# Kernel tuning notes

Hardware: AMD Instinct MI355X
Metric: run time of the kernel (lower is better)

## Reference

```python
import jax, jax.numpy as jnp
import numpy as np

B, P1, P2 = 16, 25, 24          # batch, patch-grid rows (+cls row), cols
E0, E1, E2 = 8, 8, 16           # 3-way factorized embed dim (total 1024)
H1, H2, H3 = 2, 2, 4            # 3-way head split (16 heads)
X, Y, Z = E0 // H1, E1 // H2, E2 // H3   # per-head factor dims (4,4,4)
SCALE = float((X * Y * Z) ** -0.5)        # head_dim = 64


def _tcl(x, w0, w1, w2, b):
    # Tensor Contraction Layer: mode-wise linear maps on the 3 embed modes.
    return jnp.einsum('bpqxyz,ax,cy,dz->bpqacd', x, w0, w1, w2) + b


def setup_inputs() -> dict:
    key = jax.random.key(0)
    ks = jax.random.split(key, 17)
    inp = {"x": jax.random.normal(ks[0], (B, P1, P2, E0, E1, E2), jnp.float32)}
    i = 1
    for nm in ("q", "k", "v", "o"):
        inp[f"{nm}_w0"] = jax.random.normal(ks[i], (E0, E0), jnp.float32) * (E0 ** -0.5); i += 1
        inp[f"{nm}_w1"] = jax.random.normal(ks[i], (E1, E1), jnp.float32) * (E1 ** -0.5); i += 1
        inp[f"{nm}_w2"] = jax.random.normal(ks[i], (E2, E2), jnp.float32) * (E2 ** -0.5); i += 1
        inp[f"{nm}_b"] = jax.random.normal(ks[i], (E0, E1, E2), jnp.float32) * 0.02; i += 1
    return inp


def _split_heads(t):
    t = t.reshape(B, P1, P2, X, H1, Y, H2, Z, H3)
    return t.transpose(0, 1, 2, 4, 6, 8, 3, 5, 7)


def reference(x,
              q_w0, q_w1, q_w2, q_b,
              k_w0, k_w1, k_w2, k_b,
              v_w0, v_w1, v_w2, v_b,
              o_w0, o_w1, o_w2, o_b):
    q = _tcl(x, q_w0, q_w1, q_w2, q_b)
    k = _tcl(x, k_w0, k_w1, k_w2, k_b)
    v = _tcl(x, v_w0, v_w1, v_w2, v_b)
    Q, K, V = _split_heads(q), _split_heads(k), _split_heads(v)
    # scores over all (p1,p2) x (m,n) token pairs, per (h1,h2,h3) head
    attn = jnp.einsum('bpqdefxyz,bmndefxyz->bdefpqmn', Q, K) * SCALE
    a = attn.reshape(B, H1, H2, H3, P1, P2, P1 * P2)
    a = jax.nn.softmax(a, axis=-1).reshape(attn.shape)
    out = jnp.einsum('bdefpqmn,bmndefxyz->bdefpqxyz', a, V)
    # b h1 h2 h3 p q x y z -> b p q (x h1)(y h2)(z h3)
    out = out.transpose(0, 4, 5, 6, 1, 7, 2, 8, 3).reshape(B, P1, P2, E0, E1, E2)
    return _tcl(out, o_w0, o_w1, o_w2, o_b)
```

## Files before the change

### kernel.cpp

```cpp
#include <hip/hip_runtime.h>

#define S   600
#define NB  16
#define NH  16
#define HD  64
#define QSCALE 0.18033688011112042f

#define LDT 20

typedef _Float16 f16x8 __attribute__((ext_vector_type(8)));
typedef __fp16 fp16x2 __attribute__((ext_vector_type(2)));
typedef float f32x4 __attribute__((ext_vector_type(4)));
typedef float f32x16 __attribute__((ext_vector_type(16)));
typedef int v2i __attribute__((ext_vector_type(2)));
typedef unsigned int u32;

__global__ __launch_bounds__(256) void tcl_qkv_kernel(
    const float* __restrict__ x,
    const float* __restrict__ qw0, const float* __restrict__ qw1,
    const float* __restrict__ qw2, const float* __restrict__ qb,
    const float* __restrict__ kw0, const float* __restrict__ kw1,
    const float* __restrict__ kw2, const float* __restrict__ kb,
    const float* __restrict__ vw0, const float* __restrict__ vw1,
    const float* __restrict__ vw2, const float* __restrict__ vb,
    _Float16* __restrict__ Qh, _Float16* __restrict__ Kh,
    _Float16* __restrict__ Vh)
{
  __shared__ __align__(16) float t1s[4][64 * LDT];
  __shared__ __align__(16) float t2s[4][64 * LDT];

  const int tid = threadIdx.x;
  const int wv = tid >> 6, lane = tid & 63;
  const int tok = blockIdx.x * 4 + wv;
  const int b = tok / S, t = tok - b * S;
  const int q = lane >> 3, zp = lane & 7;
  float* __restrict__ t1 = t1s[wv];
  float* __restrict__ t2 = t2s[wv];

  float2 xc[8];
  #pragma unroll
  for (int xx = 0; xx < 8; ++xx)
    xc[xx] = *(const float2*)&x[(size_t)tok * 1024 + xx * 128 + q * 16 + zp * 2];

  const int xs = lane >> 4;
  const int h1 = (lane >> 3) & 1;
  const int cc = lane & 7;
  const int ys = cc >> 1, h2 = cc & 1;

  const float* W0[3] = {qw0, kw0, vw0};
  const float* W1[3] = {qw1, kw1, vw1};
  const float* W2[3] = {qw2, kw2, vw2};
  const float* BB[3] = {qb, kb, vb};
  _Float16* OUT[3] = {Qh, Kh, Vh};

  #pragma unroll
  for (int p = 0; p < 3; ++p) {
    const float* __restrict__ w0 = W0[p];
    const float* __restrict__ w1 = W1[p];
    const float* __restrict__ w2 = W2[p];
    const float* __restrict__ bb = BB[p];
    _Float16* __restrict__ op = OUT[p];

    #pragma unroll
    for (int a = 0; a < 8; ++a) {
      float2 r = make_float2(0.f, 0.f);
      #pragma unroll
      for (int xx = 0; xx < 8; ++xx) {
        const float w = w0[a * 8 + xx];
        r.x = fmaf(w, xc[xx].x, r.x);
        r.y = fmaf(w, xc[xx].y, r.y);
      }
      *(float2*)&t1[(a * 8 + q) * LDT + zp * 2] = r;
    }
    __builtin_amdgcn_wave_barrier();

    float2 t1r[8];
    #pragma unroll
    for (int y = 0; y < 8; ++y)
      t1r[y] = *(float2*)&t1[(q * 8 + y) * LDT + zp * 2];
    #pragma unroll
    for (int c = 0; c < 8; ++c) {
      float2 r = make_float2(0.f, 0.f);
      #pragma unroll
      for (int y = 0; y < 8; ++y) {
        const float w = w1[c * 8 + y];
        r.x = fmaf(w, t1r[y].x, r.x);
        r.y = fmaf(w, t1r[y].y, r.y);
      }
      *(float2*)&t2[(q * 8 + c) * LDT + zp * 2] = r;
    }
    __builtin_amdgcn_wave_barrier();

    float t2r[16];
    #pragma unroll
    for (int k = 0; k < 4; ++k)
      *(float4*)&t2r[k * 4] = *(float4*)&t2[lane * LDT + k * 4];
    float bias[16];
    #pragma unroll
    for (int k = 0; k < 4; ++k)
      *(float4*)&bias[k * 4] = *(const float4*)&bb[lane * 16 + k * 4];
    float o[16];
    #pragma unroll
    for (int d = 0; d < 16; ++d) {
      float acc = 0.f;
      #pragma unroll
      for (int j = 0; j < 16; ++j)
        acc = fmaf(w2[d * 16 + j], t2r[j], acc);
      o[d] = acc + bias[d];
    }
    const float sc = (p == 0) ? QSCALE : 1.0f;
    #pragma unroll
    for (int h3 = 0; h3 < 4; ++h3) {
      union { _Float16 hh[4]; uint2 u; } pk;
      #pragma unroll
      for (int z = 0; z < 4; ++z)
        pk.hh[z] = (_Float16)(o[4 * z + h3] * sc);
      const int head = h1 * 8 + h2 * 4 + h3;
      *(uint2*)&op[((size_t)((b * NH + head) * S + t)) * HD + xs * 16 + ys * 4]
          = pk.u;
    }
    __builtin_amdgcn_wave_barrier();
  }
}

__global__ __launch_bounds__(256) void vtrans_kernel(
    const _Float16* __restrict__ Vh, _Float16* __restrict__ Vt)
{
  __shared__ __align__(16) _Float16 tile[64 * 64];
  const int tid = threadIdx.x;
  const int tt = blockIdx.x, h = blockIdx.y, b = blockIdx.z;
  const size_t rbase = (size_t)(b * NH + h) * S * HD;
  const size_t wbase = (size_t)(b * NH + h) * HD * S;
  const int t0 = tt * 64;

  #pragma unroll
  for (int hp = 0; hp < 2; ++hp) {
    const int u = hp * 256 + tid;
    const int r = u >> 3, ch = u & 7;
    f16x8 v = {0, 0, 0, 0, 0, 0, 0, 0};
    if (t0 + r < S) v = *(const f16x8*)&Vh[rbase + (size_t)(t0 + r) * HD + ch * 8];
    *(f16x8*)&tile[r * 64 + ((ch ^ ((r ^ (r >> 3)) & 7)) * 8)] = v;
  }
  __syncthreads();
  #pragma unroll
  for (int hp = 0; hp < 2; ++hp) {
    const int w = hp * 256 + tid;
    const int d = w >> 3, tc = w & 7;
    if (t0 + tc * 8 + 8 <= S) {
      const int cd = d >> 3;
      union { _Float16 hh[8]; f16x8 v; } g;
      #pragma unroll
      for (int e = 0; e < 8; ++e) {
        const int r = tc * 8 + e;
        g.hh[e] = tile[r * 64 + ((cd ^ ((r ^ (r >> 3)) & 7)) * 8) + (d & 7)];
      }
      *(f16x8*)&Vt[wbase + (size_t)d * S + t0 + tc * 8] = g.v;
    }
  }
}

__device__ __forceinline__ void gload16(const _Float16* g, _Float16* l) {
  __builtin_amdgcn_global_load_lds(
      (const __attribute__((address_space(1))) unsigned int*)g,
      (__attribute__((address_space(3))) unsigned int*)l, 16, 0, 0);
}

__device__ __forceinline__ u32 pk2(float lo, float hi) {
  union { fp16x2 h; u32 u; } c;
  c.h = __builtin_amdgcn_cvt_pkrtz(lo, hi);
  return c.u;
}

__device__ __forceinline__ f16x8 pfrag(u32 A0, u32 A1, u32 B0, u32 B1) {
  const v2i r = __builtin_amdgcn_permlane32_swap((int)A0, (int)B0, false, false);
  const v2i s = __builtin_amdgcn_permlane32_swap((int)A1, (int)B1, false, false);
  union { u32 w[4]; f16x8 v; } u;
  u.w[0] = (u32)r[0]; u.w[1] = (u32)s[0];
  u.w[2] = (u32)r[1]; u.w[3] = (u32)s[1];
  return u.v;
}

#define ZERO16 {0.f,0.f,0.f,0.f,0.f,0.f,0.f,0.f,0.f,0.f,0.f,0.f,0.f,0.f,0.f,0.f}

template<bool TAIL>
__device__ __forceinline__ void attn_step32(
    const _Float16* __restrict__ Ks, const _Float16* __restrict__ Vs,
    const f16x8 (&qf)[4],
    f32x16 (&po)[2], float& mrow, float& lrow,
    const int lq, const int lh)
{
  f32x16 a0 = ZERO16, a1 = ZERO16;
  __builtin_amdgcn_s_setprio(1);
  #pragma unroll
  for (int kc = 0; kc < 4; ++kc) {
    const int chb = (kc * 2 + lh) * 512;
    const f16x8 k0 = *(const f16x8*)&Ks[chb + lq * 8];
    a0 = __builtin_amdgcn_mfma_f32_32x32x16_f16(k0, qf[kc], a0, 0, 0, 0);
    if (!TAIL) {
      const f16x8 k1 = *(const f16x8*)&Ks[chb + 256 + lq * 8];
      a1 = __builtin_amdgcn_mfma_f32_32x32x16_f16(k1, qf[kc], a1, 0, 0, 0);
    }
  }
  __builtin_amdgcn_s_setprio(0);
  float sv0[16], sv1[16];
  float tmax = -1e30f;
  #pragma unroll
  for (int r = 0; r < 16; ++r) {
    float s = a0[r];
    if (TAIL && r >= 12) s = -1e30f;
    sv0[r] = s;
    tmax = fmaxf(tmax, s);
  }
  if (!TAIL) {
    #pragma unroll
    for (int r = 0; r < 16; ++r) { sv1[r] = a1[r]; tmax = fmaxf(tmax, sv1[r]); }
  }
  tmax = fmaxf(tmax, __shfl_xor(tmax, 32));
  if (!__all(tmax - mrow <= 11.0f)) {
    const float mn = fmaxf(mrow, tmax);
    const float corr = __builtin_amdgcn_exp2f(mrow - mn);
    lrow *= corr;
    po[0] *= corr;
    po[1] *= corr;
    mrow = mn;
  }
  float rs = 0.f;
  {
    float e[16];
    #pragma unroll
    for (int r = 0; r < 16; ++r) {
      e[r] = __builtin_amdgcn_exp2f(sv0[r] - mrow);
      rs += e[r];
    }
    f16x8 pf0 = pfrag(pk2(e[0], e[1]),  pk2(e[2], e[3]),
                      pk2(e[4], e[5]),  pk2(e[6], e[7]));
    f16x8 pf1 = pfrag(pk2(e[8], e[9]),  pk2(e[10], e[11]),
                      pk2(e[12], e[13]), pk2(e[14], e[15]));
    __builtin_amdgcn_s_setprio(1);
    #pragma unroll
    for (int kc2 = 0; kc2 < 2; ++kc2) {
      const f16x8 pf = kc2 ? pf1 : pf0;
      const int ch = 2 * kc2 + lh;
      #pragma unroll
      for (int db = 0; db < 2; ++db) {
        const f16x8 vf = *(const f16x8*)&Vs[ch * 512 + (db * 32 + lq) * 8];
        po[db] = __builtin_amdgcn_mfma_f32_32x32x16_f16(vf, pf, po[db], 0, 0, 0);
      }
    }
    __builtin_amdgcn_s_setprio(0);
  }
  if (!TAIL) {
    float e[16];
    #pragma unroll
    for (int r = 0; r < 16; ++r) {
      e[r] = __builtin_amdgcn_exp2f(sv1[r] - mrow);
      rs += e[r];
    }
    f16x8 pf0 = pfrag(pk2(e[0], e[1]),  pk2(e[2], e[3]),
                      pk2(e[4], e[5]),  pk2(e[6], e[7]));
    f16x8 pf1 = pfrag(pk2(e[8], e[9]),  pk2(e[10], e[11]),
                      pk2(e[12], e[13]), pk2(e[14], e[15]));
    __builtin_amdgcn_s_setprio(1);
    #pragma unroll
    for (int kc2 = 0; kc2 < 2; ++kc2) {
      const f16x8 pf = kc2 ? pf1 : pf0;
      const int ch = 2 * kc2 + lh;
      #pragma unroll
      for (int db = 0; db < 2; ++db) {
        const f16x8 vf = *(const f16x8*)&Vs[(4 + ch) * 512 + (db * 32 + lq) * 8];
        po[db] = __builtin_amdgcn_mfma_f32_32x32x16_f16(vf, pf, po[db], 0, 0, 0);
      }
    }
    __builtin_amdgcn_s_setprio(0);
  }
  rs += __shfl_xor(rs, 32);
  lrow += rs;
}

__global__ __launch_bounds__(256, 4) void attn_mfma_kernel(
    const _Float16* __restrict__ Qh, const _Float16* __restrict__ Kh,
    const _Float16* __restrict__ Vt, float* __restrict__ Og)
{
  __shared__ __align__(16) union {
    struct {
      _Float16 K[2][8 * 512];
      _Float16 V[2][8 * 512];
    } m;
    float ot[4][32 * 68];
  } sm;

  const int tid = threadIdx.x;
  const int lane = tid & 63;
  const int wv = tid >> 6;
  const int id = blockIdx.x;
  const int idx = id >> 3;
  const int bh = (id & 7) * 32 + idx / 5;
  const int qt = idx - (idx / 5) * 5;
  const size_t base  = (size_t)bh * S * HD;
  const size_t vbase = (size_t)bh * HD * S;
  const int lq = lane & 31;
  const int lh = lane >> 5;

  const int qrow_l = qt * 128 + wv * 32 + lq;
  const int qrow = (qrow_l < S) ? qrow_l : (S - 1);
  f16x8 qf[4];
  #pragma unroll
  for (int kc = 0; kc < 4; ++kc)
    qf[kc] = *(const f16x8*)&Qh[base + (size_t)qrow * HD + kc * 16 + lh * 8];

  f32x16 po[2] = {ZERO16, ZERO16};
  float mrow = -1e30f, lrow = 0.f;

  const _Float16* kg = Kh + base + (size_t)lane * HD + wv * 8;
  const _Float16* vg = Vt + vbase + (size_t)lane * S + wv * 8;

  auto gload_tile = [&](int kt, int b) {
    const _Float16* kp = kg + (size_t)kt * 64 * HD;
    const _Float16* vp = vg + kt * 64;
    gload16(kp,      &sm.m.K[b][wv * 512]);
    gload16(kp + 32, &sm.m.K[b][(wv + 4) * 512]);
    gload16(vp,      &sm.m.V[b][wv * 512]);
    gload16(vp + 32, &sm.m.V[b][(wv + 4) * 512]);
  };

  gload_tile(0, 0);
  #pragma unroll 2
  for (int kt = 0; kt < 9; ++kt) {
    const int b = kt & 1;
    __syncthreads();
    gload_tile(kt + 1, b ^ 1);
    attn_step32<false>(&sm.m.K[b][0], &sm.m.V[b][0],
                       qf, po, mrow, lrow, lq, lh);
  }
  __syncthreads();
  if (tid < 64)
    *(f16x8*)&sm.m.V[1][3 * 512 + tid * 8] = (f16x8){0,0,0,0,0,0,0,0};
  __syncthreads();
  attn_step32<true>(&sm.m.K[1][0], &sm.m.V[1][0],
                    qf, po, mrow, lrow, lq, lh);
  __syncthreads();

  const float invl = 1.0f / lrow;
  float* otw = &sm.ot[wv][0];
  #pragma unroll
  for (int db = 0; db < 2; ++db)
    #pragma unroll
    for (int g = 0; g < 4; ++g) {
      float4 v;
      v.x = po[db][4*g]   * invl;
      v.y = po[db][4*g+1] * invl;
      v.z = po[db][4*g+2] * invl;
      v.w = po[db][4*g+3] * invl;
      *(float4*)&otw[lq * 68 + db * 32 + g * 8 + lh * 4] = v;
    }
  __builtin_amdgcn_wave_barrier();
  {
    const int r = lane >> 1, half = lane & 1;
    const int gq = qt * 128 + wv * 32 + r;
    if (gq < S) {
      #pragma unroll
      for (int k2 = 0; k2 < 8; ++k2) {
        const float4 v = *(float4*)&otw[r * 68 + half * 32 + k2 * 4];
        *(float4*)&Og[base + (size_t)gq * HD + half * 32 + k2 * 4] = v;
      }
    }
  }
}

__global__ __launch_bounds__(256) void tcl_out_kernel(
    const float* __restrict__ Og,
    const float* __restrict__ ow0, const float* __restrict__ ow1,
    const float* __restrict__ ow2, const float* __restrict__ ob,
    float* __restrict__ out)
{
  __shared__ __align__(16) float t1s[4][64 * LDT];
  __shared__ __align__(16) float t2s[4][64 * LDT];

  const int tid = threadIdx.x;
  const int wv = tid >> 6, lane = tid & 63;
  const int tok = blockIdx.x * 4 + wv;
  const int b = tok / S, t = tok - b * S;
  const int q = lane >> 3, zp = lane & 7;
  float* __restrict__ t1 = t1s[wv];
  float* __restrict__ t2 = t2s[wv];

  float2 xc[8];
  {
    const int h2g = q & 1, yg = q >> 1;
    const int h3g = 2 * (zp & 1), zg = zp >> 1;
    #pragma unroll
    for (int xx = 0; xx < 8; ++xx) {
      const int headb = (xx & 1) * 8 + h2g * 4 + h3g;
      const size_t off = ((size_t)((b * NH + headb) * S + t)) * HD
                       + (xx >> 1) * 16 + yg * 4 + zg;
      xc[xx].x = Og[off];
      xc[xx].y = Og[off + (size_t)S * HD];
    }
  }

  #pragma unroll
  for (int a = 0; a < 8; ++a) {
    float2 r = make_float2(0.f, 0.f);
    #pragma unroll
    for (int xx = 0; xx < 8; ++xx) {
      const float w = ow0[a * 8 + xx];
      r.x = fmaf(w, xc[xx].x, r.x);
      r.y = fmaf(w, xc[xx].y, r.y);
    }
    *(float2*)&t1[(a * 8 + q) * LDT + zp * 2] = r;
  }
  __builtin_amdgcn_wave_barrier();

  float2 t1r[8];
  #pragma unroll
  for (int y = 0; y < 8; ++y)
    t1r[y] = *(float2*)&t1[(q * 8 + y) * LDT + zp * 2];
  #pragma unroll
  for (int c = 0; c < 8; ++c) {
    float2 r = make_float2(0.f, 0.f);
    #pragma unroll
    for (int y = 0; y < 8; ++y) {
      const float w = ow1[c * 8 + y];
      r.x = fmaf(w, t1r[y].x, r.x);
      r.y = fmaf(w, t1r[y].y, r.y);
    }
    *(float2*)&t2[(q * 8 + c) * LDT + zp * 2] = r;
  }
  __builtin_amdgcn_wave_barrier();

  float t2r[16];
  #pragma unroll
  for (int k = 0; k < 4; ++k)
    *(float4*)&t2r[k * 4] = *(float4*)&t2[lane * LDT + k * 4];
  float bias[16];
  #pragma unroll
  for (int k = 0; k < 4; ++k)
    *(float4*)&bias[k * 4] = *(const float4*)&ob[lane * 16 + k * 4];
  float o[16];
  #pragma unroll
  for (int d = 0; d < 16; ++d) {
    float acc = 0.f;
    #pragma unroll
    for (int j = 0; j < 16; ++j)
      acc = fmaf(ow2[d * 16 + j], t2r[j], acc);
    o[d] = acc + bias[d];
  }
  #pragma unroll
  for (int k = 0; k < 4; ++k) {
    const float4 res = make_float4(o[4 * k], o[4 * k + 1],
                                   o[4 * k + 2], o[4 * k + 3]);
    *(float4*)&out[(size_t)tok * 1024 + lane * 16 + k * 4] = res;
  }
}

extern "C" void kernel_launch(void* const* d_in, const int* in_sizes, int n_in,
                              void* d_out, int out_size, void* d_ws, size_t ws_size,
                              hipStream_t stream) {
  const float* x   = (const float*)d_in[0];
  const float* qw0 = (const float*)d_in[1];
  const float* qw1 = (const float*)d_in[2];
  const float* qw2 = (const float*)d_in[3];
  const float* qb  = (const float*)d_in[4];
  const float* kw0 = (const float*)d_in[5];
  const float* kw1 = (const float*)d_in[6];
  const float* kw2 = (const float*)d_in[7];
  const float* kb  = (const float*)d_in[8];
  const float* vw0 = (const float*)d_in[9];
  const float* vw1 = (const float*)d_in[10];
  const float* vw2 = (const float*)d_in[11];
  const float* vb  = (const float*)d_in[12];
  const float* ow0 = (const float*)d_in[13];
  const float* ow1 = (const float*)d_in[14];
  const float* ow2 = (const float*)d_in[15];
  const float* ob  = (const float*)d_in[16];

  const size_t N = (size_t)NB * NH * S * HD;
  _Float16* Qh  = (_Float16*)d_ws;
  _Float16* Kh  = Qh + N;
  _Float16* Vth = Kh + N;
  _Float16* Vh  = Vth + N;
  float*    O   = (float*)Vh;

  tcl_qkv_kernel<<<dim3(NB * S / 4), 256, 0, stream>>>(
      x, qw0, qw1, qw2, qb, kw0, kw1, kw2, kb, vw0, vw1, vw2, vb, Qh, Kh, Vh);
  vtrans_kernel<<<dim3(10, NH, NB), 256, 0, stream>>>(Vh, Vth);
  attn_mfma_kernel<<<dim3(1280), 256, 0, stream>>>(Qh, Kh, Vth, O);
  tcl_out_kernel<<<dim3(NB * S / 4), 256, 0, stream>>>(O, ow0, ow1, ow2, ob,
                                                       (float*)d_out);
}
```

Before: 114.1 us.

## Tree-reduce softmax max/sum, raise attention occupancy, write output directly

Replaces the serial max and sum chains in the online softmax with balanced trees, shortening their dependency chains. Removes the shared-memory staging buffer and the extra barrier in the attention epilogue, so each lane writes its normalized float4 results straight to global memory. This shrinks LDS use, and the launch bound is raised from 4 to 5 blocks per CU. The direct stores are less coalesced, and the tighter register budget could cause spills.

```diff
diff --git a/kernel.cpp b/kernel.cpp
--- a/kernel.cpp
+++ b/kernel.cpp
@@ -180,6 +180,23 @@
   return u.v;
 }
 
+__device__ __forceinline__ float max16t(const float* s) {
+  const float a0 = fmaxf(s[0], s[1]),  a1 = fmaxf(s[2], s[3]);
+  const float a2 = fmaxf(s[4], s[5]),  a3 = fmaxf(s[6], s[7]);
+  const float a4 = fmaxf(s[8], s[9]),  a5 = fmaxf(s[10], s[11]);
+  const float a6 = fmaxf(s[12], s[13]), a7 = fmaxf(s[14], s[15]);
+  const float b0 = fmaxf(a0, a1), b1 = fmaxf(a2, a3);
+  const float b2 = fmaxf(a4, a5), b3 = fmaxf(a6, a7);
+  return fmaxf(fmaxf(b0, b1), fmaxf(b2, b3));
+}
+__device__ __forceinline__ float sum16t(const float* s) {
+  const float a0 = s[0] + s[1],  a1 = s[2] + s[3];
+  const float a2 = s[4] + s[5],  a3 = s[6] + s[7];
+  const float a4 = s[8] + s[9],  a5 = s[10] + s[11];
+  const float a6 = s[12] + s[13], a7 = s[14] + s[15];
+  return ((a0 + a1) + (a2 + a3)) + ((a4 + a5) + (a6 + a7));
+}
+
 #define ZERO16 {0.f,0.f,0.f,0.f,0.f,0.f,0.f,0.f,0.f,0.f,0.f,0.f,0.f,0.f,0.f,0.f}
 
 template<bool TAIL>
@@ -203,17 +220,17 @@
   }
   __builtin_amdgcn_s_setprio(0);
   float sv0[16], sv1[16];
-  float tmax = -1e30f;
   #pragma unroll
   for (int r = 0; r < 16; ++r) {
     float s = a0[r];
     if (TAIL && r >= 12) s = -1e30f;
     sv0[r] = s;
-    tmax = fmaxf(tmax, s);
-  }
+  }
+  float tmax = max16t(sv0);
   if (!TAIL) {
     #pragma unroll
-    for (int r = 0; r < 16; ++r) { sv1[r] = a1[r]; tmax = fmaxf(tmax, sv1[r]); }
+    for (int r = 0; r < 16; ++r) sv1[r] = a1[r];
+    tmax = fmaxf(tmax, max16t(sv1));
   }
   tmax = fmaxf(tmax, __shfl_xor(tmax, 32));
   if (!__all(tmax - mrow <= 11.0f)) {
@@ -228,10 +245,9 @@
   {
     float e[16];
     #pragma unroll
-    for (int r = 0; r < 16; ++r) {
+    for (int r = 0; r < 16; ++r)
       e[r] = __builtin_amdgcn_exp2f(sv0[r] - mrow);
-      rs += e[r];
-    }
+    rs = sum16t(e);
     f16x8 pf0 = pfrag(pk2(e[0], e[1]),  pk2(e[2], e[3]),
                       pk2(e[4], e[5]),  pk2(e[6], e[7]));
     f16x8 pf1 = pfrag(pk2(e[8], e[9]),  pk2(e[10], e[11]),
@@ -252,10 +268,9 @@
   if (!TAIL) {
     float e[16];
     #pragma unroll
-    for (int r = 0; r < 16; ++r) {
+    for (int r = 0; r < 16; ++r)
       e[r] = __builtin_amdgcn_exp2f(sv1[r] - mrow);
-      rs += e[r];
-    }
+    rs += sum16t(e);
     f16x8 pf0 = pfrag(pk2(e[0], e[1]),  pk2(e[2], e[3]),
                       pk2(e[4], e[5]),  pk2(e[6], e[7]));
     f16x8 pf1 = pfrag(pk2(e[8], e[9]),  pk2(e[10], e[11]),
@@ -277,16 +292,13 @@
   lrow += rs;
 }
 
-__global__ __launch_bounds__(256, 4) void attn_mfma_kernel(
+__global__ __launch_bounds__(256, 5) void attn_mfma_kernel(
     const _Float16* __restrict__ Qh, const _Float16* __restrict__ Kh,
     const _Float16* __restrict__ Vt, float* __restrict__ Og)
 {
-  __shared__ __align__(16) union {
-    struct {
-      _Float16 K[2][8 * 512];
-      _Float16 V[2][8 * 512];
-    } m;
-    float ot[4][32 * 68];
+  __shared__ __align__(16) struct {
+    _Float16 K[2][8 * 512];
+    _Float16 V[2][8 * 512];
   } sm;
 
   const int tid = threadIdx.x;
@@ -317,10 +329,10 @@
   auto gload_tile = [&](int kt, int b) {
     const _Float16* kp = kg + (size_t)kt * 64 * HD;
     const _Float16* vp = vg + kt * 64;
-    gload16(kp,      &sm.m.K[b][wv * 512]);
-    gload16(kp + 32, &sm.m.K[b][(wv + 4) * 512]);
-    gload16(vp,      &sm.m.V[b][wv * 512]);
-    gload16(vp + 32, &sm.m.V[b][(wv + 4) * 512]);
+    gload16(kp,      &sm.K[b][wv * 512]);
+    gload16(kp + 32, &sm.K[b][(wv + 4) * 512]);
+    gload16(vp,      &sm.V[b][wv * 512]);
+    gload16(vp + 32, &sm.V[b][(wv + 4) * 512]);
   };
 
   gload_tile(0, 0);
@@ -329,41 +341,31 @@
     const int b = kt & 1;
     __syncthreads();
     gload_tile(kt + 1, b ^ 1);
-    attn_step32<false>(&sm.m.K[b][0], &sm.m.V[b][0],
+    attn_step32<false>(&sm.K[b][0], &sm.V[b][0],
                        qf, po, mrow, lrow, lq, lh);
   }
   __syncthreads();
   if (tid < 64)
-    *(f16x8*)&sm.m.V[1][3 * 512 + tid * 8] = (f16x8){0,0,0,0,0,0,0,0};
+    *(f16x8*)&sm.V[1][3 * 512 + tid * 8] = (f16x8){0,0,0,0,0,0,0,0};
   __syncthreads();
-  attn_step32<true>(&sm.m.K[1][0], &sm.m.V[1][0],
+  attn_step32<true>(&sm.K[1][0], &sm.V[1][0],
                     qf, po, mrow, lrow, lq, lh);
-  __syncthreads();
 
   const float invl = 1.0f / lrow;
-  float* otw = &sm.ot[wv][0];
-  #pragma unroll
-  for (int db = 0; db < 2; ++db)
-    #pragma unroll
-    for (int g = 0; g < 4; ++g) {
-      float4 v;
-      v.x = po[db][4*g]   * invl;
-      v.y = po[db][4*g+1] * invl;
-      v.z = po[db][4*g+2] * invl;
-      v.w = po[db][4*g+3] * invl;
-      *(float4*)&otw[lq * 68 + db * 32 + g * 8 + lh * 4] = v;
-    }
-  __builtin_amdgcn_wave_barrier();
-  {
-    const int r = lane >> 1, half = lane & 1;
-    const int gq = qt * 128 + wv * 32 + r;
-    if (gq < S) {
-      #pragma unroll
-      for (int k2 = 0; k2 < 8; ++k2) {
-        const float4 v = *(float4*)&otw[r * 68 + half * 32 + k2 * 4];
-        *(float4*)&Og[base + (size_t)gq * HD + half * 32 + k2 * 4] = v;
-      }
-    }
+  const int gq = qt * 128 + wv * 32 + lq;
+  if (gq < S) {
+    float* orow = &Og[base + (size_t)gq * HD];
+    #pragma unroll
+    for (int db = 0; db < 2; ++db)
+      #pragma unroll
+      for (int g = 0; g < 4; ++g) {
+        float4 v;
+        v.x = po[db][4*g]   * invl;
+        v.y = po[db][4*g+1] * invl;
+        v.z = po[db][4*g+2] * invl;
+        v.w = po[db][4*g+3] * invl;
+        *(float4*)&orow[db * 32 + g * 8 + lh * 4] = v;
+      }
   }
 }
 
```

Measured after the change: 204.2 us. 1.79x slower.
